# Kernel optimization log

Measured on AMD Instinct MI355X. Metric: run time of the kernel, lower is better.

The kernel has to match this reference:

```python
import jax, jax.numpy as jnp
import numpy as np

B, Q, K, D, H = 4, 2048, 2048, 512, 8
HD = D // H
_INF = -1e30


def setup_inputs() -> dict:
    key = jax.random.key(0)
    ks = jax.random.split(key, 8)
    scale = 1.0 / HD ** 0.5
    return {
        "query": jax.random.normal(ks[0], (B, Q, D), jnp.float32),
        "key": jax.random.normal(ks[1], (B, K, D), jnp.float32),
        "value": jax.random.normal(ks[2], (B, K, D), jnp.float32),
        "Wq": jax.random.normal(ks[3], (D, D), jnp.float32) * scale,  # [out,in]
        "Wk": jax.random.normal(ks[4], (D, D), jnp.float32) * scale,
        "Wv": jax.random.normal(ks[5], (D, D), jnp.float32) * scale,
        "Wo": jax.random.normal(ks[6], (D, D), jnp.float32) * scale,
        "attn_mask": jax.random.randint(ks[7], (B, K), 0, 2, jnp.int32),
    }


def reference(query, key, value, Wq, Wk, Wv, Wo, attn_mask):
    bsz, qlen, _ = query.shape
    klen = key.shape[1]
    head_q = (query @ Wq.T).reshape(bsz, qlen, H, HD)
    head_k = (key @ Wk.T).reshape(bsz, klen, H, HD)
    head_v = (value @ Wv.T).reshape(bsz, klen, H, HD)
    scale = 1.0 / HD ** 0.5
    # [b, i, j, n] score tensor, as in the torch einsum 'bind,bjnd->bijn'
    attn_score = jnp.einsum('bind,bjnd->bijn', head_q, head_k) * scale
    mask = (attn_mask == 0)[:, None, :, None]  # dim-2 mask branch
    attn_score = jnp.where(mask, _INF, attn_score)
    attn_prob = jax.nn.softmax(attn_score, axis=2)  # softmax over key axis j
    attn_vec = jnp.einsum('bijn,bjnd->bind', attn_prob, head_v)
    attn_vec = attn_vec.reshape(bsz, qlen, H * HD)
    return attn_vec @ Wo.T
```

## Files before the change

kernel.cpp:

```cpp
#include <hip/hip_runtime.h>

constexpr int Bc   = 4;
constexpr int Qlen = 2048;
constexpr int Klen = 2048;
constexpr int Dm   = 512;
constexpr int Hh   = 8;
constexpr int HDim = 64;
constexpr float C1 = 0.125f * 1.4426950408889634f;

typedef __attribute__((ext_vector_type(8))) short short8;
typedef __attribute__((ext_vector_type(8))) _Float16 half8;
typedef __attribute__((ext_vector_type(2))) __fp16 fp16x2;
typedef __attribute__((ext_vector_type(4))) float f32x4;

__device__ __forceinline__ f32x4 MFMA16(short8 a, short8 b, f32x4 c) {
  return __builtin_amdgcn_mfma_f32_16x16x32_f16(
      __builtin_bit_cast(half8, a), __builtin_bit_cast(half8, b), c, 0, 0, 0);
}

__device__ __forceinline__ void gload_lds16(const void* g, void* l) {
  __builtin_amdgcn_global_load_lds(
      (const __attribute__((address_space(1))) void*)g,
      (__attribute__((address_space(3))) void*)l, 16, 0, 0);
}

__device__ __forceinline__ unsigned short f2h(float f) {
  _Float16 h = (_Float16)f;
  return __builtin_bit_cast(unsigned short, h);
}

__device__ __forceinline__ unsigned pk2h(float a, float b) {
  fp16x2 h = __builtin_amdgcn_cvt_pkrtz(a, b);
  return __builtin_bit_cast(unsigned, h);
}

__global__ __launch_bounds__(256) void scan_mask(
    const int* __restrict__ msk, int* __restrict__ idx, int* __restrict__ cnt) {
  const int b = blockIdx.x;
  const int tid = threadIdx.x;
  __shared__ int wtot[4];
  const int* mrow = msk + b * Klen;
  int m8[8];
  int c = 0;
#pragma unroll
  for (int i = 0; i < 8; ++i) {
    m8[i] = mrow[tid * 8 + i];
    c += (m8[i] != 0);
  }
  int pre = c;
#pragma unroll
  for (int off = 1; off < 64; off <<= 1) {
    int t = __shfl_up(pre, off);
    if ((tid & 63) >= off) pre += t;
  }
  const int w = tid >> 6;
  if ((tid & 63) == 63) wtot[w] = pre;
  __syncthreads();
  int base = 0;
  for (int i = 0; i < w; ++i) base += wtot[i];
  int p = base + pre - c;
#pragma unroll
  for (int i = 0; i < 8; ++i)
    if (m8[i] != 0) idx[b * Klen + (p++)] = tid * 8 + i;
  if (tid == 255) cnt[b] = base + pre;
}

__global__ __launch_bounds__(256) void cvt4(
    const float* __restrict__ s0, const float* __restrict__ s1,
    const float* __restrict__ s2, const float* __restrict__ s3,
    unsigned short* __restrict__ o0, unsigned short* __restrict__ o1,
    unsigned short* __restrict__ o2, unsigned short* __restrict__ o3,
    const int* __restrict__ msk, float* __restrict__ biasf) {
  const int seg = blockIdx.y;
  int i = (blockIdx.x * 256 + threadIdx.x) * 4;
  if (seg < 4) {
    const float* s = (seg == 0) ? s0 : (seg == 1) ? s1 : (seg == 2) ? s2 : s3;
    unsigned short* o = (seg == 0) ? o0 : (seg == 1) ? o1 : (seg == 2) ? o2 : o3;
    float4 x = *(const float4*)(s + i);
    unsigned t[2] = {pk2h(x.x, x.y), pk2h(x.z, x.w)};
    *(uint2*)(o + i) = *(const uint2*)t;
  } else if (i + 3 < Bc * Klen) {
    int4 m = *(const int4*)(msk + i);
    float4 bo;
    bo.x = (m.x == 0) ? -60000.0f : 0.0f;
    bo.y = (m.y == 0) ? -60000.0f : 0.0f;
    bo.z = (m.z == 0) ? -60000.0f : 0.0f;
    bo.w = (m.w == 0) ? -60000.0f : 0.0f;
    *(float4*)(biasf + i) = bo;
  }
}

__global__ __launch_bounds__(256) void cvt_in(
    const float* __restrict__ q, const float* __restrict__ k,
    const float* __restrict__ v,
    unsigned short* __restrict__ qh, unsigned short* __restrict__ kh,
    unsigned short* __restrict__ vh,
    const int* __restrict__ idx, const int* __restrict__ cnt) {
  const int seg = blockIdx.y;
  int g = blockIdx.x * 256 + threadIdx.x;
  int i = g * 4;
  if (seg == 0) {
    float4 x = *(const float4*)(q + i);
    unsigned t[2] = {pk2h(x.x, x.y), pk2h(x.z, x.w)};
    *(uint2*)(qh + i) = *(const uint2*)t;
    return;
  }
  const float* s = (seg == 1) ? k : v;
  unsigned short* o = (seg == 1) ? kh : vh;
  int row = i >> 9, col = i & 511;
  int b = row >> 11, jc = row & 2047;
  int cb = cnt[b];
  if (jc < cb) {
    int j = idx[b * Klen + jc];
    float4 x = *(const float4*)(s + ((size_t)(b * Klen + j)) * 512 + col);
    unsigned t[2] = {pk2h(x.x, x.y), pk2h(x.z, x.w)};
    *(uint2*)(o + (size_t)row * 512 + col) = *(const uint2*)t;
  } else if (jc < ((cb + 127) & ~127)) {
    uint2 z = {0u, 0u};
    *(uint2*)(o + (size_t)row * 512 + col) = z;
  }
}

template <bool F16A>
__global__ __launch_bounds__(256) void gemm_qkv(
    const float* __restrict__ q_in,
    const float* __restrict__ k_in,
    const float* __restrict__ v_in,
    const unsigned short* __restrict__ qh,
    const unsigned short* __restrict__ kh,
    const unsigned short* __restrict__ vh,
    const unsigned short* __restrict__ Wqh,
    const unsigned short* __restrict__ Wkh,
    const unsigned short* __restrict__ Wvh,
    unsigned short* __restrict__ Qp,
    unsigned short* __restrict__ Kp,
    unsigned short* __restrict__ Vp,
    const int* __restrict__ cnt) {
  __shared__ unsigned short As[2][128 * 32];
  __shared__ unsigned short Bs[2][128 * 32];
  const int tid = threadIdx.x;
  const int w = tid >> 6, l = tid & 63;
  const int quad = l >> 4, l15 = l & 15;
  const int m0 = blockIdx.x * 128;
  const int n0 = blockIdx.y * 128;
  const int seg = n0 >> 9;
  const int f0  = n0 & 511;
  if constexpr (F16A) {
    if (seg != 0) {
      int local = m0 & 2047;
      if (local >= ((cnt[m0 >> 11] + 63) & ~63)) return;
    }
  }
  const float* Af = (seg == 0) ? q_in : (seg == 1) ? k_in : v_in;
  const unsigned short* Ah = (seg == 0) ? qh : (seg == 1) ? kh : vh;
  const unsigned short* W = (seg == 0) ? Wqh : (seg == 1) ? Wkh : Wvh;
  unsigned short* dst = (seg == 0) ? Qp : (seg == 1) ? Kp : Vp;

  f32x4 acc[4][4] = {};
  const int lrow = l >> 2;
  const int lcol = (l & 3) * 8;
  const int wm = (w >> 1) * 64, wn = (w & 1) * 64;

  auto stage = [&](int bs, int kk) {
#pragma unroll
    for (int i = 0; i < 2; ++i) {
      int row = w * 32 + i * 16 + lrow;
      if constexpr (F16A) {
        gload_lds16(Ah + (size_t)(m0 + row) * 512 + kk + lcol, &As[bs][row * 32 + lcol]);
      } else {
        const float* ap = Af + (size_t)(m0 + row) * 512 + kk + lcol;
        float4 x0 = *(const float4*)(ap);
        float4 x1 = *(const float4*)(ap + 4);
        unsigned t[4] = {pk2h(x0.x, x0.y), pk2h(x0.z, x0.w),
                         pk2h(x1.x, x1.y), pk2h(x1.z, x1.w)};
        *(uint4*)&As[bs][row * 32 + lcol] = *(const uint4*)t;
      }
      gload_lds16(W + (size_t)(f0 + row) * 512 + kk + lcol, &Bs[bs][row * 32 + lcol]);
    }
  };

  stage(0, 0);
  for (int kk = 0; kk < 512; kk += 32) {
    const int cur = (kk >> 5) & 1;
    __syncthreads();
    if (kk + 32 < 512) stage(cur ^ 1, kk + 32);
    short8 af[4], bf[4];
#pragma unroll
    for (int t = 0; t < 4; ++t)
      af[t] = *(const short8*)&As[cur][(wm + t * 16 + l15) * 32 + quad * 8];
#pragma unroll
    for (int t = 0; t < 4; ++t)
      bf[t] = *(const short8*)&Bs[cur][(wn + t * 16 + l15) * 32 + quad * 8];
#pragma unroll
    for (int mt = 0; mt < 4; ++mt)
#pragma unroll
      for (int nt = 0; nt < 4; ++nt)
        acc[mt][nt] = MFMA16(af[mt], bf[nt], acc[mt][nt]);
  }
  const float oscale = (seg == 0) ? C1 : 1.0f;
#pragma unroll
  for (int mt = 0; mt < 4; ++mt)
#pragma unroll
    for (int nt = 0; nt < 4; ++nt)
#pragma unroll
      for (int r = 0; r < 4; ++r) {
        int m  = m0 + wm + mt * 16 + quad * 4 + r;
        int nn = f0 + wn + nt * 16 + l15;
        int b = m >> 11, qq = m & 2047;
        int h = nn >> 6, hd = nn & 63;
        dst[(((size_t)(b * Hh + h)) * Qlen + qq) * HDim + hd] =
            f2h(acc[mt][nt][r] * oscale);
      }
}

__global__ __launch_bounds__(256) void transpose_v(
    const unsigned short* __restrict__ Vp, unsigned short* __restrict__ Vt,
    const int* __restrict__ cnt) {
  __shared__ unsigned short t[64 * 72];
  const int bh = blockIdx.y, jt = blockIdx.x;
  if (cnt) {
    if (jt * 64 >= ((cnt[bh >> 3] + 63) & ~63)) return;
  }
  const int tid = threadIdx.x;
#pragma unroll
  for (int i = 0; i < 2; ++i) {
    int g = i * 256 + tid;
    int j = g >> 3, c8 = g & 7;
    *(uint4*)&t[j * 72 + c8 * 8] =
        *(const uint4*)(Vp + ((size_t)bh * Klen + jt * 64 + j) * 64 + c8 * 8);
  }
  __syncthreads();
#pragma unroll
  for (int i = 0; i < 2; ++i) {
    int g = i * 256 + tid;
    int d = g >> 3, j8 = g & 7;
    unsigned short tmp[8];
#pragma unroll
    for (int kx = 0; kx < 8; ++kx) tmp[kx] = t[(j8 * 8 + kx) * 72 + d];
    *(uint4*)(Vt + ((size_t)bh * HDim + d) * Klen + jt * 64 + j8 * 8) = *(const uint4*)tmp;
  }
}

__global__ __launch_bounds__(256) void gemm_out(
    const unsigned short* __restrict__ Oa,
    const unsigned short* __restrict__ Woh,
    float* __restrict__ out) {
  __shared__ unsigned short As[2][128 * 32];
  __shared__ unsigned short Bs[2][128 * 32];
  const int tid = threadIdx.x;
  const int w = tid >> 6, l = tid & 63;
  const int quad = l >> 4, l15 = l & 15;
  const int m0 = blockIdx.x * 128;
  const int n0 = blockIdx.y * 128;

  f32x4 acc[4][4] = {};
  const int lrow = l >> 2;
  const int lcol = (l & 3) * 8;
  const int wm = (w >> 1) * 64, wn = (w & 1) * 64;

  auto stage = [&](int bs, int kk) {
#pragma unroll
    for (int i = 0; i < 2; ++i) {
      int row = w * 32 + i * 16 + lrow;
      gload_lds16(Oa + (size_t)(m0 + row) * 512 + kk + lcol, &As[bs][row * 32 + lcol]);
      gload_lds16(Woh + (size_t)(n0 + row) * 512 + kk + lcol, &Bs[bs][row * 32 + lcol]);
    }
  };

  stage(0, 0);
  for (int kk = 0; kk < 512; kk += 32) {
    const int cur = (kk >> 5) & 1;
    __syncthreads();
    if (kk + 32 < 512) stage(cur ^ 1, kk + 32);
    short8 af[4], bf[4];
#pragma unroll
    for (int t = 0; t < 4; ++t)
      af[t] = *(const short8*)&As[cur][(wm + t * 16 + l15) * 32 + quad * 8];
#pragma unroll
    for (int t = 0; t < 4; ++t)
      bf[t] = *(const short8*)&Bs[cur][(wn + t * 16 + l15) * 32 + quad * 8];
#pragma unroll
    for (int mt = 0; mt < 4; ++mt)
#pragma unroll
      for (int nt = 0; nt < 4; ++nt)
        acc[mt][nt] = MFMA16(af[mt], bf[nt], acc[mt][nt]);
  }
#pragma unroll
  for (int mt = 0; mt < 4; ++mt)
#pragma unroll
    for (int nt = 0; nt < 4; ++nt)
#pragma unroll
      for (int r = 0; r < 4; ++r) {
        int m  = m0 + wm + mt * 16 + quad * 4 + r;
        int nn = n0 + wn + nt * 16 + l15;
        out[(size_t)m * 512 + nn] = acc[mt][nt][r];
      }
}

template <bool KSPLIT, bool COMPACT>
__global__ __launch_bounds__(256, 4) void attn(
    const unsigned short* __restrict__ Qp,
    const unsigned short* __restrict__ Kp,
    const unsigned short* __restrict__ Vt,
    const float* __restrict__ biasf,
    const int* __restrict__ cntArr,
    unsigned short* __restrict__ Oa,
    unsigned short* __restrict__ Op,
    float* __restrict__ Sp) {
  __shared__ unsigned short Ks[2][64 * 64];
  __shared__ unsigned short Vs[2][64 * 64];
  __shared__ unsigned short Ps[4][16 * 72];

  const int tid = threadIdx.x;
  const int w = tid >> 6, l = tid & 63;
  const int quad = l >> 4, l15 = l & 15;
  const int bid = blockIdx.x;
  const int bh = bid & 31;
  const int b = bh >> 3, h = bh & 7;

  int cnt, KT;
  if constexpr (COMPACT) {
    cnt = cntArr[b];
    KT = (cnt + 63) >> 6;
  } else {
    cnt = Klen;
    KT = Klen / 64;
  }

  int qt, part, kt0, ktN;
  if constexpr (KSPLIT) {
    int rest = bid >> 5;
    part = rest & 1;
    qt = rest >> 1;
    int half = (KT + 1) >> 1;
    kt0 = part ? half : 0;
    ktN = part ? KT : half;
  } else {
    part = 0; qt = bid >> 5; kt0 = 0; ktN = KT;
  }
  const int x = l15 & 7;
  const int qrow = qt * 64 + w * 16 + l15;

  short8 aq[2];
#pragma unroll
  for (int k2 = 0; k2 < 2; ++k2)
    aq[k2] = *(const short8*)(Qp + ((size_t)bh * Qlen + qrow) * HDim + (k2 * 4 + quad) * 8);

  short8 ones;
#pragma unroll
  for (int j = 0; j < 8; ++j) ones[j] = (short)0x3C00;

  f32x4 o[4] = {};
  f32x4 o5 = {};
  float m_run = -1.0e6f;
  const float* brow = biasf + b * Klen;

  auto stage = [&](int bs, int kt) {
#pragma unroll
    for (int i = 0; i < 2; ++i) {
      int g = i * 256 + tid;
      int row = g >> 3, c8 = g & 7;
      int sb = (c8 ^ (row & 7)) * 8;
      gload_lds16(Kp + ((size_t)bh * Klen + kt * 64 + row) * HDim + sb, &Ks[bs][g * 8]);
      gload_lds16(Vt + ((size_t)bh * HDim + row) * Klen + kt * 64 + sb, &Vs[bs][g * 8]);
    }
  };

  stage(0, kt0);
  for (int kt = kt0; kt < ktN; ++kt) {
    const int cur = (kt - kt0) & 1;
    __syncthreads();
    if (kt + 1 < ktN) stage(cur ^ 1, kt + 1);

    float4 bb[4];
    if constexpr (!COMPACT) {
#pragma unroll
      for (int ct = 0; ct < 4; ++ct)
        bb[ct] = *(const float4*)(brow + kt * 64 + ct * 16 + quad * 4);
    }

    f32x4 sv[4];
    __builtin_amdgcn_s_setprio(1);
#pragma unroll
    for (int ct = 0; ct < 4; ++ct) {
      const short8 bk0 = *(const short8*)&Ks[cur][(ct * 16 + l15) * 64 + (quad ^ x) * 8];
      const short8 bk1 = *(const short8*)&Ks[cur][(ct * 16 + l15) * 64 + ((4 + quad) ^ x) * 8];
      f32x4 a = {};
      a = MFMA16(bk0, aq[0], a);
      a = MFMA16(bk1, aq[1], a);
      sv[ct] = a;
    }
    __builtin_amdgcn_s_setprio(0);

    if constexpr (!COMPACT) {
#pragma unroll
      for (int ct = 0; ct < 4; ++ct)
#pragma unroll
        for (int r = 0; r < 4; ++r)
          sv[ct][r] += bb[ct][r];
    } else {
      if (kt == KT - 1) {
#pragma unroll
        for (int ct = 0; ct < 4; ++ct)
#pragma unroll
          for (int r = 0; r < 4; ++r)
            if (kt * 64 + ct * 16 + quad * 4 + r >= cnt) sv[ct][r] = -60000.0f;
      }
    }

    float mx0 = fmaxf(fmaxf(sv[0][0], sv[0][1]), fmaxf(sv[0][2], sv[0][3]));
    float mx1 = fmaxf(fmaxf(sv[1][0], sv[1][1]), fmaxf(sv[1][2], sv[1][3]));
    float mx2 = fmaxf(fmaxf(sv[2][0], sv[2][1]), fmaxf(sv[2][2], sv[2][3]));
    float mx3 = fmaxf(fmaxf(sv[3][0], sv[3][1]), fmaxf(sv[3][2], sv[3][3]));
    float mx = fmaxf(fmaxf(mx0, mx1), fmaxf(mx2, mx3));
    mx = fmaxf(mx, __shfl_xor(mx, 16));
    mx = fmaxf(mx, __shfl_xor(mx, 32));
    if (__any(mx > m_run + 8.0f)) {
      float mnew  = fmaxf(m_run, mx);
      float alpha = exp2f(m_run - mnew);
      m_run = mnew;
#pragma unroll
      for (int ctd = 0; ctd < 4; ++ctd) o[ctd] *= alpha;
      o5 *= alpha;
    }

#pragma unroll
    for (int ct = 0; ct < 4; ++ct) {
      float p0 = exp2f(sv[ct][0] - m_run);
      float p1 = exp2f(sv[ct][1] - m_run);
      float p2 = exp2f(sv[ct][2] - m_run);
      float p3 = exp2f(sv[ct][3] - m_run);
      unsigned pk[2] = {pk2h(p0, p1), pk2h(p2, p3)};
      *(uint2*)&Ps[w][l15 * 72 + ct * 16 + quad * 4] = *(const uint2*)pk;
    }
    const short8 ap0 = *(const short8*)&Ps[w][l15 * 72 + quad * 8];
    const short8 ap1 = *(const short8*)&Ps[w][l15 * 72 + 32 + quad * 8];

    __builtin_amdgcn_s_setprio(1);
    o5 = MFMA16(ones, ap0, o5);
    o5 = MFMA16(ones, ap1, o5);
#pragma unroll
    for (int ctd = 0; ctd < 4; ++ctd) {
      const short8 bv0 = *(const short8*)&Vs[cur][(ctd * 16 + l15) * 64 + (quad ^ x) * 8];
      const short8 bv1 = *(const short8*)&Vs[cur][(ctd * 16 + l15) * 64 + ((4 + quad) ^ x) * 8];
      o[ctd] = MFMA16(bv0, ap0, o[ctd]);
      o[ctd] = MFMA16(bv1, ap1, o[ctd]);
    }
    __builtin_amdgcn_s_setprio(0);
  }

  float lt = o5[0];
  float rl = (lt > 0.0f) ? 1.0f / lt : 0.0f;
  if constexpr (KSPLIT) {
    const size_t pbase = ((size_t)part * 32 + bh) * Qlen;
    const size_t obase = (pbase + qrow) * 64;
#pragma unroll
    for (int ctd = 0; ctd < 4; ++ctd) {
      unsigned pk[2] = {pk2h(o[ctd][0] * rl, o[ctd][1] * rl),
                        pk2h(o[ctd][2] * rl, o[ctd][3] * rl)};
      *(uint2*)(Op + obase + ctd * 16 + quad * 4) = *(const uint2*)pk;
    }
    if (l < 16)
      Sp[pbase + qrow] = (lt > 0.0f) ? m_run + log2f(lt) : -1.0e30f;
  } else {
    const size_t obase = ((size_t)(b * Qlen) + qrow) * Dm + h * 64;
#pragma unroll
    for (int ctd = 0; ctd < 4; ++ctd) {
      unsigned pk[2] = {pk2h(o[ctd][0] * rl, o[ctd][1] * rl),
                        pk2h(o[ctd][2] * rl, o[ctd][3] * rl)};
      *(uint2*)(Oa + obase + ctd * 16 + quad * 4) = *(const uint2*)pk;
    }
  }
}

__global__ __launch_bounds__(256) void reduce_o(
    const unsigned short* __restrict__ Op, const float* __restrict__ Sp,
    unsigned short* __restrict__ Oa) {
  int g = blockIdx.x * 256 + threadIdx.x;
  int row = g >> 3, c8 = g & 7;
  const size_t PART = (size_t)32 * Qlen;
  float s1 = Sp[row], s2 = Sp[PART + row];
  float M = fmaxf(s1, s2);
  float w1 = exp2f(s1 - M), w2 = exp2f(s2 - M);
  float rs = 1.0f / (w1 + w2);
  w1 *= rs; w2 *= rs;
  short8 a = *(const short8*)(Op + (size_t)row * 64 + c8 * 8);
  short8 bvec = *(const short8*)(Op + (PART + row) * 64 + c8 * 8);
  half8 af = __builtin_bit_cast(half8, a);
  half8 bf = __builtin_bit_cast(half8, bvec);
  unsigned pk[4];
#pragma unroll
  for (int i = 0; i < 4; ++i) {
    float r0 = w1 * (float)af[i * 2 + 0] + w2 * (float)bf[i * 2 + 0];
    float r1 = w1 * (float)af[i * 2 + 1] + w2 * (float)bf[i * 2 + 1];
    pk[i] = pk2h(r0, r1);
  }
  int bh = row >> 11, qrow = row & 2047;
  int b = bh >> 3, h = bh & 7;
  *(uint4*)(Oa + ((size_t)(b * Qlen) + qrow) * Dm + h * 64 + c8 * 8) =
      *(const uint4*)pk;
}

extern "C" void kernel_launch(void* const* d_in, const int* in_sizes, int n_in,
                              void* d_out, int out_size, void* d_ws, size_t ws_size,
                              hipStream_t stream) {
  const float* q  = (const float*)d_in[0];
  const float* k  = (const float*)d_in[1];
  const float* v  = (const float*)d_in[2];
  const float* Wq = (const float*)d_in[3];
  const float* Wk = (const float*)d_in[4];
  const float* Wv = (const float*)d_in[5];
  const float* Wo = (const float*)d_in[6];
  const int*  msk = (const int*)d_in[7];
  float* out = (float*)d_out;

  char* ws = (char*)d_ws;
  const size_t SEG  = (size_t)Bc * Hh * Qlen * HDim * sizeof(unsigned short);
  const size_t WSEG = (size_t)Dm * Dm * sizeof(unsigned short);
  unsigned short* Qp  = (unsigned short*)(ws);
  unsigned short* Kp  = (unsigned short*)(ws + SEG);
  unsigned short* Vp  = (unsigned short*)(ws + 2 * SEG);
  unsigned short* Vt  = (unsigned short*)(ws + 3 * SEG);
  unsigned short* Oa  = Vp;
  unsigned short* Wqh = (unsigned short*)(ws + 4 * SEG);
  unsigned short* Wkh = (unsigned short*)(ws + 4 * SEG + WSEG);
  unsigned short* Wvh = (unsigned short*)(ws + 4 * SEG + 2 * WSEG);
  unsigned short* Woh = (unsigned short*)(ws + 4 * SEG + 3 * WSEG);
  int*   idxArr = (int*)(ws + 4 * SEG + 4 * WSEG);
  int*   cntArr = idxArr + Bc * Klen;
  float* Bfs    = (float*)idxArr;
  unsigned short* qh  = (unsigned short*)(ws + 4 * SEG + 4 * WSEG + 65536);
  unsigned short* kh  = qh + SEG / 2;
  unsigned short* vh  = kh + SEG / 2;
  unsigned short* Op  = qh;
  float*          Sp  = (float*)vh;
  const size_t NEED = 4 * SEG + 4 * WSEG + 65536 + 3 * SEG;
  const bool big = ws_size >= NEED;

  auto attn_split  = attn<true, true>;
  auto attn_single = attn<false, false>;

  const int wn = Dm * Dm;
  if (big) {
    hipLaunchKernelGGL(scan_mask, dim3(Bc), dim3(256), 0, stream, msk, idxArr, cntArr);
    hipLaunchKernelGGL(cvt4, dim3(wn / 1024, 4), dim3(256), 0, stream,
                       Wq, Wk, Wv, Wo, Wqh, Wkh, Wvh, Woh, msk, Bfs);
    hipLaunchKernelGGL(cvt_in, dim3(4096, 3), dim3(256), 0, stream,
                       q, k, v, qh, kh, vh, idxArr, cntArr);
    hipLaunchKernelGGL(gemm_qkv<true>, dim3(64, 12), dim3(256), 0, stream,
                       q, k, v, qh, kh, vh, Wqh, Wkh, Wvh, Qp, Kp, Vp, cntArr);
    hipLaunchKernelGGL(transpose_v, dim3(32, 32), dim3(256), 0, stream, Vp, Vt, cntArr);
    hipLaunchKernelGGL(attn_split, dim3(2048), dim3(256), 0, stream,
                       Qp, Kp, Vt, Bfs, cntArr, Oa, Op, Sp);
    hipLaunchKernelGGL(reduce_o, dim3(2048), dim3(256), 0, stream, Op, Sp, Oa);
  } else {
    hipLaunchKernelGGL(cvt4, dim3(wn / 1024, 5), dim3(256), 0, stream,
                       Wq, Wk, Wv, Wo, Wqh, Wkh, Wvh, Woh, msk, Bfs);
    hipLaunchKernelGGL(gemm_qkv<false>, dim3(64, 12), dim3(256), 0, stream,
                       q, k, v, qh, kh, vh, Wqh, Wkh, Wvh, Qp, Kp, Vp, cntArr);
    hipLaunchKernelGGL(transpose_v, dim3(32, 32), dim3(256), 0, stream, Vp, Vt,
                       (const int*)nullptr);
    hipLaunchKernelGGL(attn_single, dim3(1024), dim3(256), 0, stream,
                       Qp, Kp, Vt, Bfs, (const int*)nullptr, Oa, Op, Sp);
  }
  hipLaunchKernelGGL(gemm_out, dim3(64, 4), dim3(256), 0, stream, Oa, Woh, out);
}
```

Baseline: 197.5 us.

## Load V tiles directly into registers and drop K/V double buffering

Each thread now loads its V operand fragments for the PV MFMA straight from global memory into registers, so V no longer goes through shared memory. K keeps its LDS staging but is single-buffered, with a second barrier after the load, so the prefetch of the next tile is gone. This shrinks LDS use and removes the V LDS reads. In exchange, load latency is now exposed inside every iteration and more registers are needed, which may limit occupancy.

Result: slower. 231.0 us (+17.0%).

```diff
diff --git a/kernel.cpp b/kernel.cpp
--- a/kernel.cpp
+++ b/kernel.cpp
@@ -307,8 +307,7 @@
     unsigned short* __restrict__ Oa,
     unsigned short* __restrict__ Op,
     float* __restrict__ Sp) {
-  __shared__ unsigned short Ks[2][64 * 64];
-  __shared__ unsigned short Vs[2][64 * 64];
+  __shared__ unsigned short Ks[64 * 64];
   __shared__ unsigned short Ps[4][16 * 72];
 
   const int tid = threadIdx.x;
@@ -354,37 +353,39 @@
   f32x4 o5 = {};
   float m_run = -1.0e6f;
   const float* brow = biasf + b * Klen;
-
-  auto stage = [&](int bs, int kt) {
+  const unsigned short* vbase =
+      Vt + ((size_t)bh * HDim + l15) * Klen + quad * 8;
+
+  for (int kt = kt0; kt < ktN; ++kt) {
+    __syncthreads();
+    short8 vb0[4], vb1[4];
+#pragma unroll
+    for (int ctd = 0; ctd < 4; ++ctd) {
+      const unsigned short* p = vbase + (size_t)(ctd * 16) * Klen + kt * 64;
+      vb0[ctd] = *(const short8*)p;
+      vb1[ctd] = *(const short8*)(p + 32);
+    }
 #pragma unroll
     for (int i = 0; i < 2; ++i) {
       int g = i * 256 + tid;
       int row = g >> 3, c8 = g & 7;
       int sb = (c8 ^ (row & 7)) * 8;
-      gload_lds16(Kp + ((size_t)bh * Klen + kt * 64 + row) * HDim + sb, &Ks[bs][g * 8]);
-      gload_lds16(Vt + ((size_t)bh * HDim + row) * Klen + kt * 64 + sb, &Vs[bs][g * 8]);
-    }
-  };
-
-  stage(0, kt0);
-  for (int kt = kt0; kt < ktN; ++kt) {
-    const int cur = (kt - kt0) & 1;
-    __syncthreads();
-    if (kt + 1 < ktN) stage(cur ^ 1, kt + 1);
-
+      gload_lds16(Kp + ((size_t)bh * Klen + kt * 64 + row) * HDim + sb, &Ks[g * 8]);
+    }
     float4 bb[4];
     if constexpr (!COMPACT) {
 #pragma unroll
       for (int ct = 0; ct < 4; ++ct)
         bb[ct] = *(const float4*)(brow + kt * 64 + ct * 16 + quad * 4);
     }
+    __syncthreads();
 
     f32x4 sv[4];
     __builtin_amdgcn_s_setprio(1);
 #pragma unroll
     for (int ct = 0; ct < 4; ++ct) {
-      const short8 bk0 = *(const short8*)&Ks[cur][(ct * 16 + l15) * 64 + (quad ^ x) * 8];
-      const short8 bk1 = *(const short8*)&Ks[cur][(ct * 16 + l15) * 64 + ((4 + quad) ^ x) * 8];
+      const short8 bk0 = *(const short8*)&Ks[(ct * 16 + l15) * 64 + (quad ^ x) * 8];
+      const short8 bk1 = *(const short8*)&Ks[(ct * 16 + l15) * 64 + ((4 + quad) ^ x) * 8];
       f32x4 a = {};
       a = MFMA16(bk0, aq[0], a);
       a = MFMA16(bk1, aq[1], a);
@@ -441,10 +442,8 @@
     o5 = MFMA16(ones, ap1, o5);
 #pragma unroll
     for (int ctd = 0; ctd < 4; ++ctd) {
-      const short8 bv0 = *(const short8*)&Vs[cur][(ctd * 16 + l15) * 64 + (quad ^ x) * 8];
-      const short8 bv1 = *(const short8*)&Vs[cur][(ctd * 16 + l15) * 64 + ((4 + quad) ^ x) * 8];
-      o[ctd] = MFMA16(bv0, ap0, o[ctd]);
-      o[ctd] = MFMA16(bv1, ap1, o[ctd]);
+      o[ctd] = MFMA16(vb0[ctd], ap0, o[ctd]);
+      o[ctd] = MFMA16(vb1[ctd], ap1, o[ctd]);
     }
     __builtin_amdgcn_s_setprio(0);
   }
```
